# Kernel tuning notes

Measured on AMD Instinct MI355X. Metric: run time of the kernel, lower is better.

Reference implementation:

```python
import jax, jax.numpy as jnp
import numpy as np

THETA = 10.0      # spike threshold
TAU_SR = 10.0     # synaptic (psp) alpha-kernel time constant
TAU_REF = 1.0     # refractory alpha-kernel time constant
SCALE_REF = 2.0   # refractory kernel scale (refKernel = -2*theta*alpha)
TS = 1.0          # simulation step


def psp(x):
    """SLAYER psp: causal conv along time with alpha kernel k[n] = (n*Ts/tau)*exp(1 - n*Ts/tau),
    realized exactly as a 2-state linear IIR recurrence. x: (..., T)."""
    a = jnp.float32(np.exp(-TS / TAU_SR))
    c = jnp.float32(np.e * TS / TAU_SR)
    xt = jnp.moveaxis(x, -1, 0)  # (T, ...)
    z = jnp.zeros_like(xt[0])

    def step(carry, xin):
        p, q = carry
        q = a * q + a * p          # q[n] = sum_m x[m]*(n-m)*a^(n-m)
        p = a * p + xin            # p[n] = sum_m x[m]*a^(n-m)
        return (p, q), c * q       # k-convolution output (k[0] = 0)

    _, y = jax.lax.scan(step, (z, z), xt)
    return jnp.moveaxis(y, 0, -1)


def spike(x):
    """SLAYER spike: threshold with refractory feedback. At each step the membrane is
    psp input plus -2*theta * (alpha-kernel conv of past spikes); spike amplitude 1/Ts = 1.
    Refractory alpha kernel realized with the same 2-state IIR. x: (..., T)."""
    a = jnp.float32(np.exp(-TS / TAU_REF))
    c = jnp.float32(np.e * TS / TAU_REF)
    xt = jnp.moveaxis(x, -1, 0)
    z = jnp.zeros_like(xt[0])

    def step(carry, ut):
        p, q = carry
        q = a * q + a * p
        u = ut - SCALE_REF * THETA * c * q   # membrane = input psp + refractory response
        s = (u >= THETA).astype(ut.dtype)
        p = a * p + s                        # spike feeds refractory state (k[0]=0 so no self-effect)
        return (p, q), s

    _, y = jax.lax.scan(step, (z, z), xt)
    return jnp.moveaxis(y, 0, -1)


def conv_t(x, w, pad):
    """Per-timestep 2D conv: x (B,Cin,H,W,T), w (Cout,Cin,k,k); time folded into batch."""
    b, cin, h, wd, t = x.shape
    xt = jnp.moveaxis(x, -1, 1).reshape(b * t, cin, h, wd)
    y = jax.lax.conv_general_dilated(xt, w, (1, 1), [(pad, pad), (pad, pad)])
    y = y.reshape(b, t, y.shape[1], y.shape[2], y.shape[3])
    return jnp.moveaxis(y, 1, -1)


def pool2(x):
    """SLAYER pool: zero-pad odd dims, 2x2 sum with constant weight 1.1*theta, stride 2."""
    b, ch, h, wd, t = x.shape
    ph, pw = (-h) % 2, (-wd) % 2
    x = jnp.pad(x, ((0, 0), (0, 0), (0, ph), (0, pw), (0, 0)))
    h2, w2 = (h + ph) // 2, (wd + pw) // 2
    x = x.reshape(b, ch, h2, 2, w2, 2, t).sum(axis=(3, 5))
    return 1.1 * THETA * x


def setup_inputs() -> dict:
    key = jax.random.key(0)
    ks = jax.random.split(key, 6)
    B, T = 4, 300
    s_in = (jax.random.uniform(ks[0], (B, 2, 34, 34, T)) < 0.03).astype(jnp.float32)
    def w(k, shape, scale):
        fan_in = int(np.prod(shape[1:]))
        return jax.random.normal(k, shape, jnp.float32) * (scale / np.sqrt(fan_in))
    return {
        "s_in": s_in,
        "Wc1": w(ks[1], (24, 2, 5, 5), 10.0),    # weightScale=10
        "Wc2": w(ks[2], (48, 24, 3, 3), 15.0),   # weightScale=15
        "Wc3": w(ks[3], (96, 48, 3, 3), 15.0),   # weightScale=15
        "Wd4a": w(ks[4], (256, 96, 5, 5), 1.0),
        "Wd4b": w(ks[5], (10, 256), 1.0),
    }


def reference(s_in, Wc1, Wc2, Wc3, Wd4a, Wd4b):
    x = spike(psp(conv_t(s_in, Wc1, 2)))                  # (B,24,34,34,T)
    x = spike(psp(pool2(x)))                              # (B,24,17,17,T)
    x = spike(psp(conv_t(x, Wc2, 1)))                     # (B,48,17,17,T)
    x = spike(psp(pool2(x)))                              # (B,48,9,9,T)
    x = spike(psp(conv_t(x, Wc3, 1)))                     # (B,96,9,9,T)
    x = spike(psp(pool2(x)))                              # (B,96,5,5,T)
    x = spike(psp(jnp.einsum('bchwt,ochw->bot', x, Wd4a)))  # (B,256,T)
    x = spike(psp(jnp.einsum('bnt,on->bot', x, Wd4b)))      # (B,10,T)
    return x
```

## Files before the change

### kernel.cpp

```cpp
#include <hip/hip_runtime.h>


#define TT 300

#define A1 0.9048374180359595f
#define C1 0.2718281828459045f
#define A2 0.36787944117144233f
#define C2 2.718281828459045f
#define KREF (20.0f * C2)
#define THETA_F 10.0f

typedef float v2f __attribute__((ext_vector_type(2)));
typedef float f32x4 __attribute__((ext_vector_type(4)));
typedef short bf16x8 __attribute__((ext_vector_type(8)));

struct IIR {
  float p1, q1, p2, q2;
  __device__ IIR() : p1(0.f), q1(0.f), p2(0.f), q2(0.f) {}
  __device__ inline float step(float xin) {
    q1 = A1 * q1 + A1 * p1;
    float y = C1 * q1;
    p1 = A1 * p1 + xin;
    q2 = A2 * q2 + A2 * p2;
    float u = y - KREF * q2;
    float s = (u >= THETA_F) ? 1.0f : 0.0f;
    p2 = A2 * p2 + s;
    return s;
  }
};

__global__ __launch_bounds__(256) void transpose_rc(const float* __restrict__ in,
                                                    float* __restrict__ out,
                                                    int R, int C) {
  __shared__ float tile[64][65];
  int c0 = blockIdx.x * 64, r0 = blockIdx.y * 64;
  int tx = threadIdx.x & 63, ty = threadIdx.x >> 6;
  for (int i = ty; i < 64; i += 4) {
    int r = r0 + i, c = c0 + tx;
    if (r < R && c < C) tile[i][tx] = in[(long)r * C + c];
  }
  __syncthreads();
  for (int i = ty; i < 64; i += 4) {
    int c = c0 + i, r = r0 + tx;
    if (c < C && r < R) out[(long)c * R + r] = tile[tx][i];
  }
}

__device__ inline unsigned rne_bf16_bits(float f) {
  unsigned u = __float_as_uint(f);
  return (u + 0x7FFFu + ((u >> 16) & 1u)) >> 16;
}
template <int CIN, int KS, int CO, int MT, int KC, int CL>
__global__ __launch_bounds__(256) void prep_mfma(const float* __restrict__ Wc,
                                                 ushort* __restrict__ Wm) {
  constexpr int K = CIN * KS * KS;
  constexpr int PLANE = MT * KC * 512;
  int i = blockIdx.x * 256 + threadIdx.x;
  if (i >= PLANE) return;
  int e = i & 7, l = (i >> 3) & 63;
  int rest = i >> 9;
  int kc = rest % KC, m = rest / KC;
  int co = m * 16 + (l & 15);
  int k = kc * 32 + (l >> 4) * 8 + e;
  float w = 0.f;
  if (k < K && co < CO) {
    int ci, dy, dx;
    if (CL) {
      ci = k % CIN;
      int r = k / CIN;
      dy = r / KS;
      dx = r % KS;
    } else {
      ci = k / (KS * KS);
      int r = k % (KS * KS);
      dy = r / KS;
      dx = r % KS;
    }
    w = Wc[((co * CIN + ci) * KS + dy) * KS + dx];
  }
  unsigned b0 = rne_bf16_bits(w);
  float f0 = __uint_as_float(b0 << 16);
  float d1 = w - f0;
  unsigned b1 = rne_bf16_bits(d1);
  float f1 = __uint_as_float(b1 << 16);
  unsigned b2 = rne_bf16_bits(d1 - f1);
  Wm[i] = (ushort)b0;
  Wm[PLANE + i] = (ushort)b1;
  Wm[2 * PLANE + i] = (ushort)b2;
}

template <int CIN, int HW, int KS, int PAD, int CO, int RS, int NW, int NSUB>
__global__ __launch_bounds__(NW * 64) void conv_mfma_d(const float* __restrict__ S,
                                                       const ushort* __restrict__ Wm,
                                                       float* __restrict__ U) {
  constexpr int PH = HW + 2 * PAD;
  constexpr int K = CIN * KS * KS;
  constexpr int KC = (K + 31) / 32;
  constexpr int MT = (CO + 15) / 16;
  constexpr int N = HW * HW;
  constexpr int NT = (N + 15) / 16;
  constexpr int NG = (NT + NSUB - 1) / NSUB;
  constexpr int TILE = CIN * PH * RS;
  constexpr int KPAD = KC * 32;
  __shared__ float lin[TILE];
  __shared__ int koff[KPAD];
  const int t = blockIdx.x, b = blockIdx.y, B = gridDim.y;
  const int tid = threadIdx.x;

  for (int i = tid; i < TILE; i += NW * 64) lin[i] = 0.f;
  for (int k = tid; k < KPAD; k += NW * 64) {
    int ci = k / (KS * KS), r = k % (KS * KS), dy = r / KS, dx = r % KS;
    koff[k] = (k < K) ? (ci * PH * RS + dy * RS + dx) : 0;
  }
  __syncthreads();
  const float* src = S + ((long)t * B + b) * (CIN * N);
  for (int i = tid; i < CIN * N; i += NW * 64) {
    int ci = i / N, r = i % N, iy = r / HW, ix = r % HW;
    lin[ci * PH * RS + (iy + PAD) * RS + ix + PAD] = src[i];
  }
  __syncthreads();

  const int lane = tid & 63;
  const int wv = tid >> 6;
  const int g = lane >> 4;
  const int col = lane & 15;

  bf16x8 af[3 * MT * KC];
#pragma unroll
  for (int f = 0; f < 3 * MT * KC; ++f)
    af[f] = *(const bf16x8*)(Wm + (long)f * 512 + lane * 8);

  for (int grp = wv; grp < NG; grp += NW) {
    const int px0 = grp * (16 * NSUB);
    bool vs[NSUB];
    int pxb[NSUB];
    bf16x8 bf[NSUB][KC];
#pragma unroll
    for (int s = 0; s < NSUB; ++s) {
      int px = px0 + s * 16 + col;
      vs[s] = px < N;
      int ppx = vs[s] ? px : 0;
      int y = ppx / HW, x = ppx % HW;
      pxb[s] = y * RS + x;
#pragma unroll
      for (int kc = 0; kc < KC; ++kc) {
        bf16x8 v;
#pragma unroll
        for (int e = 0; e < 8; ++e) {
          float val = lin[pxb[s] + koff[kc * 32 + g * 8 + e]];
          v[e] = (short)(__float_as_uint(val) >> 16);
        }
        bf[s][kc] = v;
      }
    }

#pragma unroll
    for (int m = 0; m < MT; ++m) {
      f32x4 acc[NSUB];
#pragma unroll
      for (int s = 0; s < NSUB; ++s) acc[s] = (f32x4){0.f, 0.f, 0.f, 0.f};
#pragma unroll
      for (int p = 0; p < 3; ++p) {
#pragma unroll
        for (int kc = 0; kc < KC; ++kc) {
          bf16x8 a = af[(p * MT + m) * KC + kc];
#pragma unroll
          for (int s = 0; s < NSUB; ++s)
            acc[s] = __builtin_amdgcn_mfma_f32_16x16x32_bf16(a, bf[s][kc], acc[s], 0, 0, 0);
        }
      }
      const int co0 = m * 16 + g * 4;
#pragma unroll
      for (int s = 0; s < NSUB; ++s) {
        if (vs[s]) {
          float* up = U + (((long)t * B + b) * CO + co0) * N + px0 + s * 16 + col;
#pragma unroll
          for (int j = 0; j < 4; ++j)
            if (co0 + j < CO) up[(long)j * N] = acc[s][j];
        }
      }
    }
  }
}

template <int CIN, int HW, int KS, int PAD, int CO, int CPAD, int NW, int MCHUNK>
__global__ __launch_bounds__(NW * 64) void conv_mfma_v(const float* __restrict__ S,
                                                       const ushort* __restrict__ Wm,
                                                       float* __restrict__ U) {
  constexpr int PW = HW + 2 * PAD;
  constexpr int K = CIN * KS * KS;
  constexpr int KC = (K + 31) / 32;
  constexpr int KPAD = KC * 32;
  constexpr int RMAX = (KPAD - 1) / CIN;
  constexpr int DYMAX = RMAX / KS;
  constexpr int PHA = (HW + DYMAX > PW) ? (HW + DYMAX) : PW;
  constexpr int MT = CO / 16;
  constexpr int N = HW * HW;
  constexpr int NT = (N + 15) / 16;
  constexpr int NCH = MT / MCHUNK;
  constexpr int CROWS = MCHUNK * 16;
  __shared__ ushort linb[PHA * PW * CPAD];
  __shared__ int offb[KC * 4];
  __shared__ float cst[CROWS * N];
  const int t = blockIdx.x, b = blockIdx.y, B = gridDim.y;
  const int tid = threadIdx.x;

  for (int i = tid; i < PHA * PW * CPAD / 2; i += NW * 64) ((int*)linb)[i] = 0;
  for (int i = tid; i < KC * 4; i += NW * 64) {
    int k0 = (i >> 2) * 32 + (i & 3) * 8;
    int ci0 = k0 % CIN, r0 = k0 / CIN;
    offb[i] = ((r0 / KS) * PW + (r0 % KS)) * CPAD + ci0;
  }
  __syncthreads();
  const float* src = S + ((long)t * B + b) * (CIN * N);
  for (int i = tid; i < CIN * N; i += NW * 64) {
    int ci = i / N, r = i % N, iy = r / HW, ix = r % HW;
    linb[((iy + PAD) * PW + ix + PAD) * CPAD + ci] =
        (ushort)(__float_as_uint(src[i]) >> 16);
  }
  __syncthreads();

  const int lane = tid & 63;
  const int wv = tid >> 6;
  const int g = lane >> 4;
  const int col = lane & 15;

  int boff[KC];
#pragma unroll
  for (int kc = 0; kc < KC; ++kc) boff[kc] = offb[kc * 4 + g];

  for (int ch = blockIdx.z; ch < NCH; ch += gridDim.z) {
    for (int nt = wv; nt < NT; nt += NW) {
      int px = nt * 16 + col;
      bool vpx = px < N;
      int ppx = vpx ? px : 0;
      int y = ppx / HW, x = ppx % HW;
      const int pxb = (y * PW + x) * CPAD;

      bf16x8 bf[KC];
#pragma unroll
      for (int kc = 0; kc < KC; ++kc)
        bf[kc] = *(const bf16x8*)(linb + pxb + boff[kc]);

#pragma unroll
      for (int ml = 0; ml < MCHUNK; ++ml) {
        const int m = ch * MCHUNK + ml;
        f32x4 acc = {0.f, 0.f, 0.f, 0.f};
#pragma unroll
        for (int p = 0; p < 3; ++p) {
#pragma unroll
          for (int kc = 0; kc < KC; ++kc) {
            bf16x8 a = *(const bf16x8*)(Wm + ((long)(p * MT + m) * KC + kc) * 512 + lane * 8);
            acc = __builtin_amdgcn_mfma_f32_16x16x32_bf16(a, bf[kc], acc, 0, 0, 0);
          }
        }
        if (vpx) {
          const int r0 = ml * 16 + g * 4;
#pragma unroll
          for (int j = 0; j < 4; ++j) cst[(r0 + j) * N + px] = acc[j];
        }
      }
    }
    __syncthreads();
    const f32x4* cs = (const f32x4*)cst;
    f32x4* ug = (f32x4*)(U + (((long)t * B + b) * CO + ch * CROWS) * N);
    for (int i = tid; i < CROWS * N / 4; i += NW * 64) ug[i] = cs[i];
    __syncthreads();
  }
}

template <int C, int HIN, int HOUT>
__global__ __launch_bounds__(128) void ppp4_tm(const float* __restrict__ U,
                                               float* __restrict__ out, int B) {
  const int NOUT = B * C * HOUT * HOUT;
  const long SIN = (long)B * C * HIN * HIN;
  int id = blockIdx.x * 128 + threadIdx.x;
  int sub = id & 3, m = id >> 2;
  bool active = m < NOUT;
  int mm = active ? m : 0;
  int x2 = mm % HOUT;
  int y2 = (mm / HOUT) % HOUT;
  int c = (mm / (HOUT * HOUT)) % C;
  int b = mm / (C * HOUT * HOUT);
  int iy = 2 * y2 + (sub >> 1), ix = 2 * x2 + (sub & 1);
  bool valid = active && iy < HIN && ix < HIN;
  const float* base = U + ((long)(b * C + c) * HIN + iy) * HIN + ix;
  bool writer = active && (sub == 0);
  float* op = out + mm;
  IIR si, so;
  float pr0 = valid ? base[0] : 0.f;
  float pr1 = valid ? base[SIN] : 0.f;
  float pr2 = valid ? base[2 * SIN] : 0.f;
  float pr3 = valid ? base[3 * SIN] : 0.f;
  for (int tb = 0; tb < TT; tb += 4) {
    float a0 = pr0, a1 = pr1, a2 = pr2, a3 = pr3;
    const float* nb = base + (long)(tb + 4) * SIN;
    pr0 = valid ? nb[0] : 0.f;
    pr1 = valid ? nb[SIN] : 0.f;
    pr2 = valid ? nb[2 * SIN] : 0.f;
    pr3 = valid ? nb[3 * SIN] : 0.f;
    {
      float s = si.step(a0);
      float v = s + __shfl_xor(s, 1); v += __shfl_xor(v, 2);
      float o = so.step(11.0f * v);
      if (writer) op[(long)tb * NOUT] = o;
    }
    {
      float s = si.step(a1);
      float v = s + __shfl_xor(s, 1); v += __shfl_xor(v, 2);
      float o = so.step(11.0f * v);
      if (writer) op[(long)(tb + 1) * NOUT] = o;
    }
    {
      float s = si.step(a2);
      float v = s + __shfl_xor(s, 1); v += __shfl_xor(v, 2);
      float o = so.step(11.0f * v);
      if (writer) op[(long)(tb + 2) * NOUT] = o;
    }
    {
      float s = si.step(a3);
      float v = s + __shfl_xor(s, 1); v += __shfl_xor(v, 2);
      float o = so.step(11.0f * v);
      if (writer) op[(long)(tb + 3) * NOUT] = o;
    }
  }
}

__global__ __launch_bounds__(256) void dense7k(const float* __restrict__ S,
                                               const float* __restrict__ Wt,
                                               float* __restrict__ P) {
  const int r0 = blockIdx.x * 16 + (threadIdx.x >> 6) * 4;
  const int kz = blockIdx.y;
  const int lane = threadIdx.x & 63;
  const float* s0 = S + (long)r0 * 2400;
  const float* s1 = s0 + 2400;
  const float* s2 = s0 + 4800;
  const float* s3 = s0 + 7200;
  const float* wp = Wt + lane * 4;
  v2f aA[4], aB[4];
#pragma unroll
  for (int o = 0; o < 4; ++o) { aA[o] = (v2f)(0.f); aB[o] = (v2f)(0.f); }
  const int k0 = kz * 300, k1 = k0 + 300;
  for (int k = k0; k < k1; k += 4) {
    float4 a0 = *(const float4*)(s0 + k);
    float4 a1 = *(const float4*)(s1 + k);
    float4 a2 = *(const float4*)(s2 + k);
    float4 a3 = *(const float4*)(s3 + k);
#define DSTEP(KK, AX)                                                        \
    {                                                                        \
      float4 w = *(const float4*)(wp + (long)(k + KK) * 256);                \
      v2f pA, pB;                                                            \
      pA.x = a0.AX; pA.y = a1.AX; pB.x = a2.AX; pB.y = a3.AX;                \
      aA[0] += pA * w.x; aA[1] += pA * w.y; aA[2] += pA * w.z; aA[3] += pA * w.w; \
      aB[0] += pB * w.x; aB[1] += pB * w.y; aB[2] += pB * w.z; aB[3] += pB * w.w; \
    }
    DSTEP(0, x) DSTEP(1, y) DSTEP(2, z) DSTEP(3, w)
#undef DSTEP
  }
  float* p = P + (long)kz * 307200 + (long)r0 * 256 + lane * 4;
#pragma unroll
  for (int o = 0; o < 4; ++o) p[o] = aA[o].x;
#pragma unroll
  for (int o = 0; o < 4; ++o) p[256 + o] = aA[o].y;
#pragma unroll
  for (int o = 0; o < 4; ++o) p[512 + o] = aB[o].x;
#pragma unroll
  for (int o = 0; o < 4; ++o) p[768 + o] = aB[o].y;
}

__global__ __launch_bounds__(256) void reduce8(const float* __restrict__ P,
                                               float* __restrict__ U7) {
  int i = blockIdx.x * 256 + threadIdx.x;
  if (i >= 76800) return;
  const float4* p = (const float4*)P;
  float4 a = p[i];
#pragma unroll
  for (int kz = 1; kz < 8; ++kz) {
    float4 b = p[(long)kz * 76800 + i];
    a.x += b.x; a.y += b.y; a.z += b.z; a.w += b.w;
  }
  ((float4*)U7)[i] = a;
}

__global__ __launch_bounds__(128) void psp7(const float* __restrict__ U7,
                                            float* __restrict__ out) {
  int n = blockIdx.x * 128 + threadIdx.x;
  IIR st;
  float pr0 = U7[n], pr1 = U7[1024 + n], pr2 = U7[2048 + n], pr3 = U7[3072 + n];
  for (int tb = 0; tb < TT; tb += 4) {
    float a0 = pr0, a1 = pr1, a2 = pr2, a3 = pr3;
    const float* nb = U7 + (long)(tb + 4) * 1024 + n;
    pr0 = nb[0]; pr1 = nb[1024]; pr2 = nb[2048]; pr3 = nb[3072];
    out[(long)tb * 1024 + n] = st.step(a0);
    out[(long)(tb + 1) * 1024 + n] = st.step(a1);
    out[(long)(tb + 2) * 1024 + n] = st.step(a2);
    out[(long)(tb + 3) * 1024 + n] = st.step(a3);
  }
}

__global__ __launch_bounds__(256) void dense8(const float* __restrict__ S,
                                              const float* __restrict__ W,
                                              float* __restrict__ U) {
  int id = blockIdx.x * 256 + threadIdx.x;
  if (id >= 12000) return;
  int o = id % 10, row = id / 10;
  const float* sr = S + (long)row * 256;
  const float* wr = W + o * 256;
  float acc = 0.f;
  for (int k = 0; k < 256; k += 4) {
    float4 a = *(const float4*)(sr + k);
    float4 w = *(const float4*)(wr + k);
    acc += a.x * w.x; acc += a.y * w.y; acc += a.z * w.z; acc += a.w * w.w;
  }
  U[id] = acc;
}

__global__ void psp8_out(const float* __restrict__ U, float* __restrict__ out) {
  int n = threadIdx.x;
  bool act = n < 40;
  int nn = act ? n : 0;
  IIR st;
  float pr0 = U[nn], pr1 = U[40 + nn], pr2 = U[80 + nn], pr3 = U[120 + nn];
  for (int tb = 0; tb < TT; tb += 4) {
    float a0 = pr0, a1 = pr1, a2 = pr2, a3 = pr3;
    const float* nb = U + (long)(tb + 4) * 40 + nn;
    pr0 = nb[0]; pr1 = nb[40]; pr2 = nb[80]; pr3 = nb[120];
    float o0 = st.step(a0), o1 = st.step(a1), o2 = st.step(a2), o3 = st.step(a3);
    if (act) {
      out[nn * TT + tb] = o0;
      out[nn * TT + tb + 1] = o1;
      out[nn * TT + tb + 2] = o2;
      out[nn * TT + tb + 3] = o3;
    }
  }
}

extern "C" void kernel_launch(void* const* d_in, const int* in_sizes, int n_in,
                              void* d_out, int out_size, void* d_ws, size_t ws_size,
                              hipStream_t stream) {
  const float* s_in = (const float*)d_in[0];
  const float* Wc1  = (const float*)d_in[1];
  const float* Wc2  = (const float*)d_in[2];
  const float* Wc3  = (const float*)d_in[3];
  const float* Wd4a = (const float*)d_in[4];
  const float* Wd4b = (const float*)d_in[5];

  float* Buf1 = (float*)d_ws;
  float* Buf2 = Buf1 + 33292800;
  float* s2   = Buf2;
  float* s4   = Buf2 + 8323200;
  float* Wt4a = Buf2 + 12988800;
  float* T0   = Buf2 + 13910400;
  float* s7   = Buf2 + 16737840;
  float* P7   = Buf2 + 17045040;
  float* U7   = Buf2 + 19502640;
  float* s6   = Buf2;
  float* U8   = Buf1;
  ushort* Wm1 = (ushort*)P7;
  ushort* Wm2 = Wm1 + 18432;
  ushort* Wm3 = Wm1 + 50688;

  transpose_rc<<<dim3(5, 145), 256, 0, stream>>>(s_in, T0, 9248, 300);
  transpose_rc<<<dim3(38, 4), 256, 0, stream>>>(Wd4a, Wt4a, 256, 2400);
  prep_mfma<2, 5, 24, 2, 2, 0><<<24, 256, 0, stream>>>(Wc1, Wm1);
  prep_mfma<24, 3, 48, 3, 7, 1><<<42, 256, 0, stream>>>(Wc2, Wm2);
  prep_mfma<48, 3, 96, 6, 14, 1><<<168, 256, 0, stream>>>(Wc3, Wm3);

  conv_mfma_d<2, 34, 5, 2, 24, 39, 8, 4><<<dim3(300, 4), 512, 0, stream>>>(T0, Wm1, Buf1);
  ppp4_tm<24, 34, 17><<<867, 128, 0, stream>>>(Buf1, s2, 4);
  conv_mfma_v<24, 17, 3, 1, 48, 24, 8, 1><<<dim3(300, 4), 512, 0, stream>>>(s2, Wm2, Buf1);
  ppp4_tm<48, 17, 9><<<486, 128, 0, stream>>>(Buf1, s4, 4);
  conv_mfma_v<48, 9, 3, 1, 96, 56, 6, 3><<<dim3(300, 4, 2), 384, 0, stream>>>(s4, Wm3, Buf1);
  ppp4_tm<96, 9, 5><<<300, 128, 0, stream>>>(Buf1, s6, 4);
  dense7k<<<dim3(75, 8), 256, 0, stream>>>(s6, Wt4a, P7);
  reduce8<<<300, 256, 0, stream>>>(P7, U7);
  psp7<<<8, 128, 0, stream>>>(U7, s7);
  dense8<<<47, 256, 0, stream>>>(s7, Wd4b, U8);
  psp8_out<<<1, 64, 0, stream>>>(U8, (float*)d_out);
}
```

Baseline: 554.2 us.

## Add weight-stationary MFMA conv kernel for layer 3, one wave per m-tile

Adds a conv_mfma_w kernel for the third convolution. Each wave owns one 16-row output-channel tile, loads blocks of 7 weight fragments into registers and reuses them across all pixel tiles, accumulating every pixel tile in registers. The previous launch split channels across a z-dimension of 2; the new one uses a single block per (t,b) that covers all 96 channels, so the input staging is no longer duplicated. The trade-off is fewer blocks and more registers per thread, which can lower occupancy.

```diff
diff --git a/kernel.cpp b/kernel.cpp
--- a/kernel.cpp
+++ b/kernel.cpp
@@ -267,6 +267,100 @@
     for (int i = tid; i < CROWS * N / 4; i += NW * 64) ug[i] = cs[i];
     __syncthreads();
   }
+}
+
+template <int CIN, int HW, int KS, int PAD, int CO, int CPAD, int NW>
+__global__ __launch_bounds__(NW * 64) void conv_mfma_w(const float* __restrict__ S,
+                                                       const ushort* __restrict__ Wm,
+                                                       float* __restrict__ U) {
+  constexpr int PW = HW + 2 * PAD;
+  constexpr int K = CIN * KS * KS;
+  constexpr int KC = (K + 31) / 32;
+  constexpr int KPAD = KC * 32;
+  constexpr int RMAX = (KPAD - 1) / CIN;
+  constexpr int DYMAX = RMAX / KS;
+  constexpr int PHA = (HW + DYMAX > PW) ? (HW + DYMAX) : PW;
+  constexpr int MT = CO / 16;
+  static_assert(MT == NW, "wave per m-tile");
+  constexpr int N = HW * HW;
+  constexpr int NT = (N + 15) / 16;
+  constexpr int KCB = 7;
+  constexpr int KB = KC / KCB;
+  static_assert(KC % KCB == 0, "KCB divides KC");
+  __shared__ ushort linb[PHA * PW * CPAD];
+  __shared__ int offb[KC * 4];
+  __shared__ float cst[CO * N];
+  const int t = blockIdx.x, b = blockIdx.y, B = gridDim.y;
+  const int tid = threadIdx.x;
+
+  for (int i = tid; i < PHA * PW * CPAD / 2; i += NW * 64) ((int*)linb)[i] = 0;
+  for (int i = tid; i < KC * 4; i += NW * 64) {
+    int k0 = (i >> 2) * 32 + (i & 3) * 8;
+    int ci0 = k0 % CIN, r0 = k0 / CIN;
+    offb[i] = ((r0 / KS) * PW + (r0 % KS)) * CPAD + ci0;
+  }
+  __syncthreads();
+  const float* src = S + ((long)t * B + b) * (CIN * N);
+  for (int i = tid; i < CIN * N; i += NW * 64) {
+    int ci = i / N, r = i % N, iy = r / HW, ix = r % HW;
+    linb[((iy + PAD) * PW + ix + PAD) * CPAD + ci] =
+        (ushort)(__float_as_uint(src[i]) >> 16);
+  }
+  __syncthreads();
+
+  const int lane = tid & 63;
+  const int m = tid >> 6;
+  const int g = lane >> 4;
+  const int col = lane & 15;
+
+  int boff[KC];
+#pragma unroll
+  for (int kc = 0; kc < KC; ++kc) boff[kc] = offb[kc * 4 + g];
+
+  int pxb[NT];
+#pragma unroll
+  for (int nt = 0; nt < NT; ++nt) {
+    int px = nt * 16 + col;
+    int ppx = (px < N) ? px : 0;
+    int y = ppx / HW, x = ppx % HW;
+    pxb[nt] = (y * PW + x) * CPAD;
+  }
+
+  f32x4 acc[NT];
+#pragma unroll
+  for (int nt = 0; nt < NT; ++nt) acc[nt] = (f32x4){0.f, 0.f, 0.f, 0.f};
+
+  for (int p = 0; p < 3; ++p) {
+#pragma unroll 1
+    for (int kb = 0; kb < KB; ++kb) {
+      bf16x8 af[KCB];
+#pragma unroll
+      for (int q = 0; q < KCB; ++q)
+        af[q] = *(const bf16x8*)(Wm + ((long)(p * MT + m) * KC + kb * KCB + q) * 512 + lane * 8);
+#pragma unroll 1
+      for (int nt = 0; nt < NT; ++nt) {
+#pragma unroll
+        for (int q = 0; q < KCB; ++q) {
+          bf16x8 bf = *(const bf16x8*)(linb + pxb[nt] + boff[kb * KCB + q]);
+          acc[nt] = __builtin_amdgcn_mfma_f32_16x16x32_bf16(af[q], bf, acc[nt], 0, 0, 0);
+        }
+      }
+    }
+  }
+
+  const int r0 = m * 16 + g * 4;
+#pragma unroll
+  for (int nt = 0; nt < NT; ++nt) {
+    int px = nt * 16 + col;
+    if (px < N) {
+#pragma unroll
+      for (int j = 0; j < 4; ++j) cst[(r0 + j) * N + px] = acc[nt][j];
+    }
+  }
+  __syncthreads();
+  const f32x4* cs = (const f32x4*)cst;
+  f32x4* ug = (f32x4*)(U + (((long)t * B + b) * CO) * N);
+  for (int i = tid; i < CO * N / 4; i += NW * 64) ug[i] = cs[i];
 }
 
 template <int C, int HIN, int HOUT>
@@ -470,7 +564,7 @@
   ppp4_tm<24, 34, 17><<<867, 128, 0, stream>>>(Buf1, s2, 4);
   conv_mfma_v<24, 17, 3, 1, 48, 24, 8, 1><<<dim3(300, 4), 512, 0, stream>>>(s2, Wm2, Buf1);
   ppp4_tm<48, 17, 9><<<486, 128, 0, stream>>>(Buf1, s4, 4);
-  conv_mfma_v<48, 9, 3, 1, 96, 56, 6, 3><<<dim3(300, 4, 2), 384, 0, stream>>>(s4, Wm3, Buf1);
+  conv_mfma_w<48, 9, 3, 1, 96, 56, 6><<<dim3(300, 4), 384, 0, stream>>>(s4, Wm3, Buf1);
   ppp4_tm<96, 9, 5><<<300, 128, 0, stream>>>(Buf1, s6, 4);
   dense7k<<<dim3(75, 8), 256, 0, stream>>>(s6, Wt4a, P7);
   reduce8<<<300, 256, 0, stream>>>(P7, U7);
```

Measured after the change: 579.7 us. 1.05x slower.
